# Kernel tuning notes

Measured on AMD Instinct MI355X. Metric: run time of the kernel, lower is better.

Reference implementation:

```python
import jax, jax.numpy as jnp
import numpy as np

N = 100000
F_IN = 512
HID = 16
N_CLS = 40
E = 3200000


def gcn_conv(x, W, b, src, dst, n_nodes):
    # PyG GCNConv: add self loops, symmetric deg^{-1/2} norm, linear, aggregate.
    loop = jnp.arange(n_nodes, dtype=src.dtype)
    s = jnp.concatenate([src, loop])  # [E+N]
    d = jnp.concatenate([dst, loop])
    deg = jax.ops.segment_sum(jnp.ones_like(d, dtype=x.dtype), d, num_segments=n_nodes)
    dinv = jnp.where(deg > 0, jax.lax.rsqrt(deg), 0.0)
    norm = dinv[s] * dinv[d]  # [E+N]
    h = x @ W  # [N, out] -- transform before propagate (cheaper: out <= in)
    msg = h[s] * norm[:, None]  # gather + scale
    out = jax.ops.segment_sum(msg, d, num_segments=n_nodes)  # scatter-add
    return out + b


def setup_inputs() -> dict:
    key = jax.random.key(0)
    ks = jax.random.split(key, 6)
    x = jax.random.normal(ks[0], (N, F_IN), dtype=jnp.float32)
    edge_index = jax.random.randint(ks[1], (2, E), 0, N, dtype=jnp.int64)
    W1 = jax.random.normal(ks[2], (F_IN, HID), dtype=jnp.float32) / np.sqrt(F_IN)
    b1 = jnp.zeros((HID,), dtype=jnp.float32)
    W2 = jax.random.normal(ks[3], (HID, N_CLS), dtype=jnp.float32) / np.sqrt(HID)
    b2 = jnp.zeros((N_CLS,), dtype=jnp.float32)
    return {"x": x, "edge_index": edge_index, "W1": W1, "b1": b1, "W2": W2, "b2": b2}


def reference(x, edge_index, W1, b1, W2, b2):
    src, dst = edge_index[0], edge_index[1]
    h = gcn_conv(x, W1, b1, src, dst, x.shape[0])
    h = jax.nn.relu(h)
    # dropout: eval mode (identity) for a deterministic reference
    h = gcn_conv(h, W2, b2, src, dst, x.shape[0])
    return jax.nn.log_softmax(h, axis=1)
```

## Files before the change

kernel.cpp:

```cpp
#include <hip/hip_runtime.h>

#define N_NODES 100000
#define NEDGE   3200000
#define F_IN    512
#define HID     16
#define NCLS    40

#define BSHIFT  8
#define BNODES  256
#define NBUCK   ((N_NODES + BNODES - 1) / BNODES)
#define BCAP    8832
#define EPB     5120
#define NPART   (NEDGE / EPB)

typedef __bf16 bf16x8 __attribute__((ext_vector_type(8)));
typedef float floatx4 __attribute__((ext_vector_type(4)));
typedef _Float16 f16x4 __attribute__((ext_vector_type(4)));

__global__ __launch_bounds__(256) void k_part(const int* __restrict__ src,
                                              const int* __restrict__ dst,
                                              int* __restrict__ gcnt,
                                              int* __restrict__ ebuf) {
    __shared__ int hist[NBUCK];
    int t = threadIdx.x;
    for (int i = t; i < NBUCK; i += 256) hist[i] = 0;
    __syncthreads();

    int base = blockIdx.x * EPB + t * 4;
    int4 dr[5];
    #pragma unroll
    for (int s = 0; s < 5; s++) {
        dr[s] = *(const int4*)(dst + base + s * 1024);
        atomicAdd(&hist[dr[s].x >> BSHIFT], 1);
        atomicAdd(&hist[dr[s].y >> BSHIFT], 1);
        atomicAdd(&hist[dr[s].z >> BSHIFT], 1);
        atomicAdd(&hist[dr[s].w >> BSHIFT], 1);
    }
    __syncthreads();

    for (int i = t; i < NBUCK; i += 256) {
        int h = hist[i];
        hist[i] = h ? atomicAdd(&gcnt[i], h) : 0;
    }
    __syncthreads();

    #pragma unroll
    for (int s = 0; s < 5; s++) {
        int4 s4 = *(const int4*)(src + base + s * 1024);
        int dd[4] = {dr[s].x, dr[s].y, dr[s].z, dr[s].w};
        int ss[4] = {s4.x, s4.y, s4.z, s4.w};
        #pragma unroll
        for (int j = 0; j < 4; j++) {
            int d = dd[j];
            int b = d >> BSHIFT;
            int p = atomicAdd(&hist[b], 1);
            if (p < BCAP) ebuf[b * BCAP + p] = ((d & (BNODES - 1)) << 17) | ss[j];
        }
    }
}

__global__ __launch_bounds__(256) void k_sortb(const int* __restrict__ gcnt,
                                               const int* __restrict__ ebuf,
                                               int* __restrict__ col,
                                               int* __restrict__ rinfo) {
    __shared__ int ed[BCAP];
    __shared__ int cnt[BNODES];
    __shared__ int pref[BNODES];
    int b = blockIdx.x, t = threadIdx.x;

    int partial = 0;
    for (int i = t; i < b; i += 256) partial += gcnt[i];
    pref[t] = partial;
    __syncthreads();
    for (int off = 128; off; off >>= 1) {
        if (t < off) pref[t] += pref[t + off];
        __syncthreads();
    }
    int gbase = pref[0];
    __syncthreads();

    int ne = gcnt[b];
    if (ne > BCAP) ne = BCAP;
    cnt[t] = 0;
    __syncthreads();
    for (int i = t; i < ne; i += 256) {
        int e = ebuf[b * BCAP + i];
        ed[i] = e;
        atomicAdd(&cnt[e >> 17], 1);
    }
    __syncthreads();
    int c = cnt[t];
    pref[t] = c;
    __syncthreads();
    for (int off = 1; off < 256; off <<= 1) {
        int add = (t >= off) ? pref[t - off] : 0;
        __syncthreads();
        pref[t] += add;
        __syncthreads();
    }
    int start = pref[t] - c;
    int v = b * BNODES + t;
    if (v < N_NODES) rinfo[v] = (c << 22) | (gbase + start);
    cnt[t] = start;
    __syncthreads();
    for (int i = t; i < ne; i += 256) {
        int e = ed[i];
        int pos = atomicAdd(&cnt[e >> 17], 1);
        col[gbase + pos] = e & 0x1FFFF;
    }
}

__global__ __launch_bounds__(256) void k_gemm1(const float* __restrict__ x,
                                               const float* __restrict__ W1,
                                               const int* __restrict__ rinfo,
                                               _Float16* __restrict__ h1s) {
    __shared__ __bf16 wh[16 * 64 * 8];
    __shared__ __bf16 wl[16 * 64 * 8];
    int t = threadIdx.x;
    for (int e = t; e < 8192; e += 256) {
        int c = e >> 9, l = (e >> 3) & 63, j = e & 7;
        int k = c * 32 + ((l >> 4) << 3) + j;
        int n = l & 15;
        float wv = W1[k * HID + n];
        __bf16 h = (__bf16)wv;
        wh[e] = h;
        wl[e] = (__bf16)(wv - (float)h);
    }
    __syncthreads();

    int wave = t >> 6, lane = t & 63;
    int q = lane >> 4, m = lane & 15;
    int row0 = blockIdx.x * 64 + wave * 16;
    int rowa = row0 + m;
    if (rowa >= N_NODES) rowa = N_NODES - 1;
    const float* xr = x + (size_t)rowa * F_IN + q * 8;

    floatx4 acc = {0.f, 0.f, 0.f, 0.f};
    #pragma unroll 4
    for (int c = 0; c < 16; c++) {
        float4 a0 = *(const float4*)(xr + c * 32);
        float4 a1 = *(const float4*)(xr + c * 32 + 4);
        float xv[8] = {a0.x, a0.y, a0.z, a0.w, a1.x, a1.y, a1.z, a1.w};
        bf16x8 ah, al;
        #pragma unroll
        for (int j = 0; j < 8; j++) {
            __bf16 h = (__bf16)xv[j];
            ah[j] = h;
            al[j] = (__bf16)(xv[j] - (float)h);
        }
        bf16x8 bh = *(const bf16x8*)&wh[(c * 64 + lane) * 8];
        bf16x8 bl = *(const bf16x8*)&wl[(c * 64 + lane) * 8];
        acc = __builtin_amdgcn_mfma_f32_16x16x32_bf16(ah, bh, acc, 0, 0, 0);
        acc = __builtin_amdgcn_mfma_f32_16x16x32_bf16(ah, bl, acc, 0, 0, 0);
        acc = __builtin_amdgcn_mfma_f32_16x16x32_bf16(al, bh, acc, 0, 0, 0);
    }
    #pragma unroll
    for (int r = 0; r < 4; r++) {
        int grow = row0 + q * 4 + r;
        if (grow < N_NODES) {
            float dv = rsqrtf((float)(((rinfo[grow] >> 22) & 0x3FF) + 1));
            h1s[grow * HID + (lane & 15)] = (_Float16)(dv * acc[r]);
        }
    }
}

#define ACC4(gv) { a0 += (float)gv[0]; a1 += (float)gv[1]; \
                   a2 += (float)gv[2]; a3 += (float)gv[3]; }

__global__ __launch_bounds__(256) void k_agg1(const _Float16* __restrict__ h1s,
        const int* __restrict__ rinfo, const int* __restrict__ col,
        const float* __restrict__ b1, _Float16* __restrict__ ys) {
    int g = blockIdx.x * 256 + threadIdx.x;
    int v = g >> 2, q = g & 3;
    if (v >= N_NODES) return;
    int ri = rinfo[v];
    int beg = ri & 0x3FFFFF;
    int deg = (ri >> 22) & 0x3FF;
    int end = beg + deg;
    const f16x4* tab = (const f16x4*)h1s;
    float a0 = 0.f, a1 = 0.f, a2 = 0.f, a3 = 0.f;
    int j = beg;
    for (; j + 7 < end; j += 8) {
        int c0 = col[j],     c1 = col[j + 1], c2 = col[j + 2], c3 = col[j + 3];
        int c4 = col[j + 4], c5 = col[j + 5], c6 = col[j + 6], c7 = col[j + 7];
        f16x4 g0 = tab[c0 * 4 + q], g1 = tab[c1 * 4 + q];
        f16x4 g2 = tab[c2 * 4 + q], g3 = tab[c3 * 4 + q];
        f16x4 g4 = tab[c4 * 4 + q], g5 = tab[c5 * 4 + q];
        f16x4 g6 = tab[c6 * 4 + q], g7 = tab[c7 * 4 + q];
        ACC4(g0) ACC4(g1) ACC4(g2) ACC4(g3)
        ACC4(g4) ACC4(g5) ACC4(g6) ACC4(g7)
    }
    for (; j < end; j++) {
        f16x4 gv = tab[col[j] * 4 + q];
        ACC4(gv)
    }
    f16x4 sv = tab[v * 4 + q];
    ACC4(sv)
    float dv = rsqrtf((float)(deg + 1));
    f16x4 o;
    o[0] = (_Float16)(dv * fmaxf(dv * a0 + b1[q * 4 + 0], 0.f));
    o[1] = (_Float16)(dv * fmaxf(dv * a1 + b1[q * 4 + 1], 0.f));
    o[2] = (_Float16)(dv * fmaxf(dv * a2 + b1[q * 4 + 2], 0.f));
    o[3] = (_Float16)(dv * fmaxf(dv * a3 + b1[q * 4 + 3], 0.f));
    ((f16x4*)ys)[v * 4 + q] = o;
}

__global__ __launch_bounds__(256) void k_agg2(const _Float16* __restrict__ ys,
        const int* __restrict__ rinfo, const int* __restrict__ col,
        const float* __restrict__ W2, const float* __restrict__ b2,
        float* __restrict__ out) {
    __shared__ float w2s[HID * NCLS];
    __shared__ float b2s[NCLS];
    int t = threadIdx.x;
    for (int i = t; i < HID * NCLS; i += 256) w2s[i] = W2[i];
    if (t < NCLS) b2s[t] = b2[t];
    __syncthreads();

    int g = blockIdx.x * 256 + t;
    int v = g >> 2, q = g & 3;
    if (v >= N_NODES) return;
    int ri = rinfo[v];
    int beg = ri & 0x3FFFFF;
    int deg = (ri >> 22) & 0x3FF;
    int end = beg + deg;
    const f16x4* tab = (const f16x4*)ys;
    float a0 = 0.f, a1 = 0.f, a2 = 0.f, a3 = 0.f;
    int j = beg;
    for (; j + 7 < end; j += 8) {
        int c0 = col[j],     c1 = col[j + 1], c2 = col[j + 2], c3 = col[j + 3];
        int c4 = col[j + 4], c5 = col[j + 5], c6 = col[j + 6], c7 = col[j + 7];
        f16x4 g0 = tab[c0 * 4 + q], g1 = tab[c1 * 4 + q];
        f16x4 g2 = tab[c2 * 4 + q], g3 = tab[c3 * 4 + q];
        f16x4 g4 = tab[c4 * 4 + q], g5 = tab[c5 * 4 + q];
        f16x4 g6 = tab[c6 * 4 + q], g7 = tab[c7 * 4 + q];
        ACC4(g0) ACC4(g1) ACC4(g2) ACC4(g3)
        ACC4(g4) ACC4(g5) ACC4(g6) ACC4(g7)
    }
    for (; j < end; j++) {
        f16x4 gv = tab[col[j] * 4 + q];
        ACC4(gv)
    }
    f16x4 sv = tab[v * 4 + q];
    ACC4(sv)
    float dv = rsqrtf((float)(deg + 1));
    float tv[4] = {dv * a0, dv * a1, dv * a2, dv * a3};

    float lg[10];
    #pragma unroll
    for (int i = 0; i < 10; i++) lg[i] = b2s[q * 10 + i];
    #pragma unroll
    for (int k = 0; k < 16; k++) {
        float tk = __shfl(tv[k & 3], k >> 2, 4);
        #pragma unroll
        for (int i = 0; i < 10; i++)
            lg[i] = fmaf(tk, w2s[k * NCLS + q * 10 + i], lg[i]);
    }
    float mx = lg[0];
    #pragma unroll
    for (int i = 1; i < 10; i++) mx = fmaxf(mx, lg[i]);
    mx = fmaxf(mx, __shfl_xor(mx, 1, 4));
    mx = fmaxf(mx, __shfl_xor(mx, 2, 4));
    float s = 0.f;
    #pragma unroll
    for (int i = 0; i < 10; i++) s += __expf(lg[i] - mx);
    s += __shfl_xor(s, 1, 4);
    s += __shfl_xor(s, 2, 4);
    float lse = mx + __logf(s);
    #pragma unroll
    for (int i = 0; i < 10; i++) out[v * NCLS + q * 10 + i] = lg[i] - lse;
}

extern "C" void kernel_launch(void* const* d_in, const int* in_sizes, int n_in,
                              void* d_out, int out_size, void* d_ws, size_t ws_size,
                              hipStream_t stream) {
    const float* x  = (const float*)d_in[0];
    const int*   ei = (const int*)d_in[1];
    const float* W1 = (const float*)d_in[2];
    const float* b1 = (const float*)d_in[3];
    const float* W2 = (const float*)d_in[4];
    const float* b2 = (const float*)d_in[5];
    float* out = (float*)d_out;
    const int* src = ei;
    const int* dst = ei + NEDGE;

    char* w = (char*)d_ws;
    size_t o = 0;
    auto alloc = [&](size_t bytes) -> char* {
        char* p = w + o;
        o += (bytes + 511) & ~(size_t)511;
        return p;
    };
    int*      gcnt  = (int*)alloc((size_t)NBUCK * 4);
    int*      rinfo = (int*)alloc((size_t)N_NODES * 4);
    int*      col   = (int*)alloc((size_t)NEDGE * 4);
    char*     uni   = alloc((size_t)NBUCK * BCAP * 4);
    int*      ebuf  = (int*)uni;
    _Float16* h1s   = (_Float16*)uni;
    _Float16* ys    = h1s + (size_t)N_NODES * HID;

    hipMemsetAsync(gcnt, 0, (size_t)NBUCK * 4, stream);

    k_part <<<NPART, 256, 0, stream>>>(src, dst, gcnt, ebuf);
    k_sortb<<<NBUCK, 256, 0, stream>>>(gcnt, ebuf, col, rinfo);
    k_gemm1<<<(N_NODES + 63) / 64, 256, 0, stream>>>(x, W1, rinfo, h1s);
    k_agg1 <<<(N_NODES * 4 + 255) / 256, 256, 0, stream>>>(h1s, rinfo, col, b1, ys);
    k_agg2 <<<(N_NODES * 4 + 255) / 256, 256, 0, stream>>>(ys, rinfo, col, W2, b2, out);
}
```

Measured before the change: 449.0 us.

## Run edge partitioning and layer-1 GEMM concurrently in one fused launch

Merges the edge-bucketing kernel and the x@W1 GEMM into a single launch whose blocks are split by index, so the compute-bound GEMM overlaps with the atomic-heavy partition pass. The degree normalisation, which needs degrees not yet known during the GEMM, is moved into the sort kernel as an in-place rescale of the unscaled h1 rows. This removes one kernel launch and the GEMM's dependency on the sort. In exchange, h1 and ebuf can no longer alias and need separate workspace, and h1 takes an extra read-modify-write pass with a second fp16 rounding.

```diff
diff --git a/kernel.cpp b/kernel.cpp
--- a/kernel.cpp
+++ b/kernel.cpp
@@ -12,49 +12,101 @@
 #define BCAP    8832
 #define EPB     5120
 #define NPART   (NEDGE / EPB)
+#define NGEMM   ((N_NODES + 63) / 64)
 
 typedef __bf16 bf16x8 __attribute__((ext_vector_type(8)));
 typedef float floatx4 __attribute__((ext_vector_type(4)));
 typedef _Float16 f16x4 __attribute__((ext_vector_type(4)));
 
-__global__ __launch_bounds__(256) void k_part(const int* __restrict__ src,
-                                              const int* __restrict__ dst,
-                                              int* __restrict__ gcnt,
-                                              int* __restrict__ ebuf) {
-    __shared__ int hist[NBUCK];
+__global__ __launch_bounds__(256) void k_partgemm(
+        const int* __restrict__ src, const int* __restrict__ dst,
+        int* __restrict__ gcnt, int* __restrict__ ebuf,
+        const float* __restrict__ x, const float* __restrict__ W1,
+        _Float16* __restrict__ h1u) {
+    __shared__ char smraw[32768];
     int t = threadIdx.x;
-    for (int i = t; i < NBUCK; i += 256) hist[i] = 0;
-    __syncthreads();
-
-    int base = blockIdx.x * EPB + t * 4;
-    int4 dr[5];
-    #pragma unroll
-    for (int s = 0; s < 5; s++) {
-        dr[s] = *(const int4*)(dst + base + s * 1024);
-        atomicAdd(&hist[dr[s].x >> BSHIFT], 1);
-        atomicAdd(&hist[dr[s].y >> BSHIFT], 1);
-        atomicAdd(&hist[dr[s].z >> BSHIFT], 1);
-        atomicAdd(&hist[dr[s].w >> BSHIFT], 1);
-    }
-    __syncthreads();
-
-    for (int i = t; i < NBUCK; i += 256) {
-        int h = hist[i];
-        hist[i] = h ? atomicAdd(&gcnt[i], h) : 0;
-    }
-    __syncthreads();
-
-    #pragma unroll
-    for (int s = 0; s < 5; s++) {
-        int4 s4 = *(const int4*)(src + base + s * 1024);
-        int dd[4] = {dr[s].x, dr[s].y, dr[s].z, dr[s].w};
-        int ss[4] = {s4.x, s4.y, s4.z, s4.w};
-        #pragma unroll
-        for (int j = 0; j < 4; j++) {
-            int d = dd[j];
-            int b = d >> BSHIFT;
-            int p = atomicAdd(&hist[b], 1);
-            if (p < BCAP) ebuf[b * BCAP + p] = ((d & (BNODES - 1)) << 17) | ss[j];
+
+    if (blockIdx.x < NPART) {
+        int* hist = (int*)smraw;
+        for (int i = t; i < NBUCK; i += 256) hist[i] = 0;
+        __syncthreads();
+
+        int base = blockIdx.x * EPB + t * 4;
+        int4 dr[5];
+        #pragma unroll
+        for (int s = 0; s < 5; s++) {
+            dr[s] = *(const int4*)(dst + base + s * 1024);
+            atomicAdd(&hist[dr[s].x >> BSHIFT], 1);
+            atomicAdd(&hist[dr[s].y >> BSHIFT], 1);
+            atomicAdd(&hist[dr[s].z >> BSHIFT], 1);
+            atomicAdd(&hist[dr[s].w >> BSHIFT], 1);
+        }
+        __syncthreads();
+
+        for (int i = t; i < NBUCK; i += 256) {
+            int h = hist[i];
+            hist[i] = h ? atomicAdd(&gcnt[i], h) : 0;
+        }
+        __syncthreads();
+
+        #pragma unroll
+        for (int s = 0; s < 5; s++) {
+            int4 s4 = *(const int4*)(src + base + s * 1024);
+            int dd[4] = {dr[s].x, dr[s].y, dr[s].z, dr[s].w};
+            int ss[4] = {s4.x, s4.y, s4.z, s4.w};
+            #pragma unroll
+            for (int j = 0; j < 4; j++) {
+                int d = dd[j];
+                int b = d >> BSHIFT;
+                int p = atomicAdd(&hist[b], 1);
+                if (p < BCAP) ebuf[b * BCAP + p] = ((d & (BNODES - 1)) << 17) | ss[j];
+            }
+        }
+    } else {
+        __bf16* wh = (__bf16*)smraw;
+        __bf16* wl = wh + 8192;
+        for (int e = t; e < 8192; e += 256) {
+            int c = e >> 9, l = (e >> 3) & 63, j = e & 7;
+            int k = c * 32 + ((l >> 4) << 3) + j;
+            int n = l & 15;
+            float wv = W1[k * HID + n];
+            __bf16 h = (__bf16)wv;
+            wh[e] = h;
+            wl[e] = (__bf16)(wv - (float)h);
+        }
+        __syncthreads();
+
+        int wave = t >> 6, lane = t & 63;
+        int q = lane >> 4, m = lane & 15;
+        int row0 = (blockIdx.x - NPART) * 64 + wave * 16;
+        int rowa = row0 + m;
+        if (rowa >= N_NODES) rowa = N_NODES - 1;
+        const float* xr = x + (size_t)rowa * F_IN + q * 8;
+
+        floatx4 acc = {0.f, 0.f, 0.f, 0.f};
+        #pragma unroll 4
+        for (int c = 0; c < 16; c++) {
+            float4 a0 = *(const float4*)(xr + c * 32);
+            float4 a1 = *(const float4*)(xr + c * 32 + 4);
+            float xv[8] = {a0.x, a0.y, a0.z, a0.w, a1.x, a1.y, a1.z, a1.w};
+            bf16x8 ah, al;
+            #pragma unroll
+            for (int j = 0; j < 8; j++) {
+                __bf16 h = (__bf16)xv[j];
+                ah[j] = h;
+                al[j] = (__bf16)(xv[j] - (float)h);
+            }
+            bf16x8 bh = *(const bf16x8*)&wh[(c * 64 + lane) * 8];
+            bf16x8 bl = *(const bf16x8*)&wl[(c * 64 + lane) * 8];
+            acc = __builtin_amdgcn_mfma_f32_16x16x32_bf16(ah, bh, acc, 0, 0, 0);
+            acc = __builtin_amdgcn_mfma_f32_16x16x32_bf16(ah, bl, acc, 0, 0, 0);
+            acc = __builtin_amdgcn_mfma_f32_16x16x32_bf16(al, bh, acc, 0, 0, 0);
+        }
+        #pragma unroll
+        for (int r = 0; r < 4; r++) {
+            int grow = row0 + q * 4 + r;
+            if (grow < N_NODES)
+                h1u[grow * HID + (lane & 15)] = (_Float16)acc[r];
         }
     }
 }
@@ -62,7 +114,8 @@
 __global__ __launch_bounds__(256) void k_sortb(const int* __restrict__ gcnt,
                                                const int* __restrict__ ebuf,
                                                int* __restrict__ col,
-                                               int* __restrict__ rinfo) {
+                                               int* __restrict__ rinfo,
+                                               _Float16* __restrict__ h1) {
     __shared__ int ed[BCAP];
     __shared__ int cnt[BNODES];
     __shared__ int pref[BNODES];
@@ -100,67 +153,26 @@
     }
     int start = pref[t] - c;
     int v = b * BNODES + t;
-    if (v < N_NODES) rinfo[v] = (c << 22) | (gbase + start);
+    if (v < N_NODES) {
+        rinfo[v] = (c << 22) | (gbase + start);
+        float dv = rsqrtf((float)(c + 1));
+        f16x4* row = (f16x4*)(h1 + (size_t)v * HID);
+        #pragma unroll
+        for (int r = 0; r < 4; r++) {
+            f16x4 vv = row[r];
+            vv[0] = (_Float16)(dv * (float)vv[0]);
+            vv[1] = (_Float16)(dv * (float)vv[1]);
+            vv[2] = (_Float16)(dv * (float)vv[2]);
+            vv[3] = (_Float16)(dv * (float)vv[3]);
+            row[r] = vv;
+        }
+    }
     cnt[t] = start;
     __syncthreads();
     for (int i = t; i < ne; i += 256) {
         int e = ed[i];
         int pos = atomicAdd(&cnt[e >> 17], 1);
         col[gbase + pos] = e & 0x1FFFF;
-    }
-}
-
-__global__ __launch_bounds__(256) void k_gemm1(const float* __restrict__ x,
-                                               const float* __restrict__ W1,
-                                               const int* __restrict__ rinfo,
-                                               _Float16* __restrict__ h1s) {
-    __shared__ __bf16 wh[16 * 64 * 8];
-    __shared__ __bf16 wl[16 * 64 * 8];
-    int t = threadIdx.x;
-    for (int e = t; e < 8192; e += 256) {
-        int c = e >> 9, l = (e >> 3) & 63, j = e & 7;
-        int k = c * 32 + ((l >> 4) << 3) + j;
-        int n = l & 15;
-        float wv = W1[k * HID + n];
-        __bf16 h = (__bf16)wv;
-        wh[e] = h;
-        wl[e] = (__bf16)(wv - (float)h);
-    }
-    __syncthreads();
-
-    int wave = t >> 6, lane = t & 63;
-    int q = lane >> 4, m = lane & 15;
-    int row0 = blockIdx.x * 64 + wave * 16;
-    int rowa = row0 + m;
-    if (rowa >= N_NODES) rowa = N_NODES - 1;
-    const float* xr = x + (size_t)rowa * F_IN + q * 8;
-
-    floatx4 acc = {0.f, 0.f, 0.f, 0.f};
-    #pragma unroll 4
-    for (int c = 0; c < 16; c++) {
-        float4 a0 = *(const float4*)(xr + c * 32);
-        float4 a1 = *(const float4*)(xr + c * 32 + 4);
-        float xv[8] = {a0.x, a0.y, a0.z, a0.w, a1.x, a1.y, a1.z, a1.w};
-        bf16x8 ah, al;
-        #pragma unroll
-        for (int j = 0; j < 8; j++) {
-            __bf16 h = (__bf16)xv[j];
-            ah[j] = h;
-            al[j] = (__bf16)(xv[j] - (float)h);
-        }
-        bf16x8 bh = *(const bf16x8*)&wh[(c * 64 + lane) * 8];
-        bf16x8 bl = *(const bf16x8*)&wl[(c * 64 + lane) * 8];
-        acc = __builtin_amdgcn_mfma_f32_16x16x32_bf16(ah, bh, acc, 0, 0, 0);
-        acc = __builtin_amdgcn_mfma_f32_16x16x32_bf16(ah, bl, acc, 0, 0, 0);
-        acc = __builtin_amdgcn_mfma_f32_16x16x32_bf16(al, bh, acc, 0, 0, 0);
-    }
-    #pragma unroll
-    for (int r = 0; r < 4; r++) {
-        int grow = row0 + q * 4 + r;
-        if (grow < N_NODES) {
-            float dv = rsqrtf((float)(((rinfo[grow] >> 22) & 0x3FF) + 1));
-            h1s[grow * HID + (lane & 15)] = (_Float16)(dv * acc[r]);
-        }
     }
 }
 
@@ -293,16 +305,14 @@
     int*      gcnt  = (int*)alloc((size_t)NBUCK * 4);
     int*      rinfo = (int*)alloc((size_t)N_NODES * 4);
     int*      col   = (int*)alloc((size_t)NEDGE * 4);
-    char*     uni   = alloc((size_t)NBUCK * BCAP * 4);
-    int*      ebuf  = (int*)uni;
-    _Float16* h1s   = (_Float16*)uni;
-    _Float16* ys    = h1s + (size_t)N_NODES * HID;
+    int*      ebuf  = (int*)alloc((size_t)NBUCK * BCAP * 4);
+    _Float16* h1s   = (_Float16*)alloc((size_t)N_NODES * HID * 2);
+    _Float16* ys    = (_Float16*)alloc((size_t)N_NODES * HID * 2);
 
     hipMemsetAsync(gcnt, 0, (size_t)NBUCK * 4, stream);
 
-    k_part <<<NPART, 256, 0, stream>>>(src, dst, gcnt, ebuf);
-    k_sortb<<<NBUCK, 256, 0, stream>>>(gcnt, ebuf, col, rinfo);
-    k_gemm1<<<(N_NODES + 63) / 64, 256, 0, stream>>>(x, W1, rinfo, h1s);
-    k_agg1 <<<(N_NODES * 4 + 255) / 256, 256, 0, stream>>>(h1s, rinfo, col, b1, ys);
-    k_agg2 <<<(N_NODES * 4 + 255) / 256, 256, 0, stream>>>(ys, rinfo, col, W2, b2, out);
-}
+    k_partgemm<<<NPART + NGEMM, 256, 0, stream>>>(src, dst, gcnt, ebuf, x, W1, h1s);
+    k_sortb   <<<NBUCK, 256, 0, stream>>>(gcnt, ebuf, col, rinfo, h1s);
+    k_agg1    <<<(N_NODES * 4 + 255) / 256, 256, 0, stream>>>(h1s, rinfo, col, b1, ys);
+    k_agg2    <<<(N_NODES * 4 + 255) / 256, 256, 0, stream>>>(ys, rinfo, col, W2, b2, out);
+}
```

Result: faster. 431.3 us (-3.9%).
